# Optimization experiments

Hardware: AMD Instinct MI355X
Metric: run time of the kernel (lower is better)

Reference implementation:

```python
import jax, jax.numpy as jnp
import numpy as np

B, S, D, H = 8, 1024, 1024, 16
HD = D // H  # head_dim = 64


def setup_inputs() -> dict:
    key = jax.random.key(0)
    ks = jax.random.split(key, 5)
    scale = 1.0 / np.sqrt(D)
    return {
        "x": jax.random.normal(ks[0], (B, S, D), dtype=jnp.float32),
        "wq": jax.random.normal(ks[1], (D, D), dtype=jnp.float32) * scale,
        "wk": jax.random.normal(ks[2], (D, D), dtype=jnp.float32) * scale,
        "wv": jax.random.normal(ks[3], (D, D), dtype=jnp.float32) * scale,
        "wo": jax.random.normal(ks[4], (D, D), dtype=jnp.float32) * scale,
    }


def reference(x, wq, wk, wv, wo):
    b, s, d = x.shape
    # nn.Linear: y = x @ W.T  (weights stored [out, in])
    q = (x @ wq.T).reshape(b, s, H, HD).transpose(0, 2, 1, 3)  # [b,h,s,hd]
    k = (x @ wk.T).reshape(b, s, H, HD).transpose(0, 2, 1, 3)
    v = (x @ wv.T).reshape(b, s, H, HD).transpose(0, 2, 1, 3)
    scores = jnp.einsum("bhqd,bhkd->bhqk", q, k) / jnp.sqrt(jnp.float32(HD))
    attn = jax.nn.softmax(scores, axis=-1)  # dropout p=0.0 -> identity
    out = jnp.einsum("bhqk,bhkd->bhqd", attn, v)
    out = out.transpose(0, 2, 1, 3).reshape(b, s, d)
    return out @ wo.T
```

## Files before the change

kernel.cpp:

```cpp
#include <hip/hip_runtime.h>
#include <hip/hip_bf16.h>
#include <math.h>

#define BB 8
#define SS 1024
#define DD 1024
#define HH 16
#define HDIM 64
#define MM (BB * SS)
#define QSCALE 0.1803368801111204f

typedef __attribute__((ext_vector_type(8))) short s8v;
typedef __attribute__((ext_vector_type(4))) short s4v;
typedef __attribute__((ext_vector_type(4))) float f4v;

#define GLD16(g, l)                                                            \
  __builtin_amdgcn_global_load_lds(                                            \
      (const __attribute__((address_space(1))) void*)(g),                      \
      (__attribute__((address_space(3))) void*)(l), 16, 0, 0)

__device__ __forceinline__ unsigned short bf16_ru(float f) {
  return (unsigned short)((__float_as_uint(f) + 0x8000u) >> 16);
}

__device__ __forceinline__ unsigned bf16_pack2(float f0, float f1) {
#if __has_builtin(__builtin_amdgcn_perm)
  unsigned a = __float_as_uint(f0) + 0x8000u;
  unsigned b = __float_as_uint(f1) + 0x8000u;
  return __builtin_amdgcn_perm(b, a, 0x07060302u);
#else
  return (unsigned)bf16_ru(f0) | ((unsigned)bf16_ru(f1) << 16);
#endif
}

__device__ __forceinline__ float fast_exp2(float x) {
  return __builtin_amdgcn_exp2f(x);
}

__global__ void cast_all(const float* __restrict__ x, const float* __restrict__ wq,
                         const float* __restrict__ wk, const float* __restrict__ wv,
                         const float* __restrict__ wo, __hip_bfloat16* __restrict__ xb,
                         __hip_bfloat16* __restrict__ wqkvb,
                         __hip_bfloat16* __restrict__ wob) {
  int blk = blockIdx.x;
  const float* src;
  __hip_bfloat16* dst;
  int base;
  if (blk < 2048) {
    src = x; dst = xb; base = blk * 4096;
  } else if (blk < 2304) {
    src = wq; dst = wqkvb; base = (blk - 2048) * 4096;
  } else if (blk < 2560) {
    src = wk; dst = wqkvb + (1 << 20); base = (blk - 2304) * 4096;
  } else if (blk < 2816) {
    src = wv; dst = wqkvb + (2 << 20); base = (blk - 2560) * 4096;
  } else {
    src = wo; dst = wob; base = (blk - 2816) * 4096;
  }
#pragma unroll
  for (int it = 0; it < 4; ++it) {
    int idx = base + it * 1024 + threadIdx.x * 4;
    float4 f = *(const float4*)&src[idx];
    *(uint2*)&dst[idx] = uint2{bf16_pack2(f.x, f.y), bf16_pack2(f.z, f.w)};
  }
}

template <int MODE>
__global__ __launch_bounds__(256, (MODE == 0 ? 4 : 3)) void gemm_bt(
    const __hip_bfloat16* __restrict__ A, const __hip_bfloat16* __restrict__ Bm,
    float* __restrict__ Cf, __hip_bfloat16* __restrict__ Qo,
    __hip_bfloat16* __restrict__ Ko, __hip_bfloat16* __restrict__ Vt) {
  __shared__ __hip_bfloat16 sA[128 * 64];
  __shared__ __hip_bfloat16 sB[128 * 64];

  const int tid = threadIdx.x;
  const int wave = tid >> 6;
  const int lane = tid & 63;
  const int l15 = lane & 15;
  const int quad = lane >> 4;
  const int c8 = lane & 7;
  const int r8 = lane >> 3;

  const int m0 = blockIdx.y * 128;
  const int n0 = blockIdx.x * 128;
  const int wm = (wave >> 1) * 64;
  const int wn = (wave & 1) * 64;

  f4v acc[4][4];
#pragma unroll
  for (int i = 0; i < 4; ++i)
#pragma unroll
    for (int j = 0; j < 4; ++j) acc[i][j] = {0.f, 0.f, 0.f, 0.f};

  for (int kt = 0; kt < DD / 64; ++kt) {
    const int k0 = kt * 64;
    __syncthreads();
#pragma unroll
    for (int r = 0; r < 4; ++r) {
      int rb = r * 32 + wave * 8;
      int row = rb + r8;
      int scol = (c8 ^ (row & 7)) * 8;
      GLD16(A + (size_t)(m0 + row) * DD + k0 + scol, &sA[rb * 64]);
      GLD16(Bm + (size_t)(n0 + row) * DD + k0 + scol, &sB[rb * 64]);
    }
    __syncthreads();

#pragma unroll
    for (int kk = 0; kk < 2; ++kk) {
      s8v af[4], bf[4];
#pragma unroll
      for (int i = 0; i < 4; ++i)
        af[i] = *(const s8v*)&sA[(wm + i * 16 + l15) * 64 +
                                 (((kk * 4 + quad) ^ (l15 & 7)) * 8)];
#pragma unroll
      for (int j = 0; j < 4; ++j)
        bf[j] = *(const s8v*)&sB[(wn + j * 16 + l15) * 64 +
                                 (((kk * 4 + quad) ^ (l15 & 7)) * 8)];
#pragma unroll
      for (int i = 0; i < 4; ++i)
#pragma unroll
        for (int j = 0; j < 4; ++j)
          acc[i][j] = (MODE == 2)
                          ? __builtin_amdgcn_mfma_f32_16x16x32_bf16(af[i], bf[j],
                                                                    acc[i][j], 0, 0, 0)
                          : __builtin_amdgcn_mfma_f32_16x16x32_bf16(bf[j], af[i],
                                                                    acc[i][j], 0, 0, 0);
    }
  }

#pragma unroll
  for (int i = 0; i < 4; ++i) {
#pragma unroll
    for (int j = 0; j < 4; ++j) {
      if (MODE == 0) {
        const int s_abs = m0 + wm + i * 16 + l15;
        const int col = n0 + wn + j * 16 + quad * 4;
        const bool isQ = (n0 < 1024);
        const int hcol = col & 1023;
        const int h = hcol >> 6, hd = hcol & 63;
        const int b = s_abs >> 10, s = s_abs & 1023;
        const float scl = isQ ? QSCALE : 1.0f;
        __hip_bfloat16* dst = isQ ? Qo : Ko;
        *(uint2*)&dst[((size_t)(b * HH + h) * SS + s) * HDIM + hd] =
            uint2{bf16_pack2(acc[i][j][0] * scl, acc[i][j][1] * scl),
                  bf16_pack2(acc[i][j][2] * scl, acc[i][j][3] * scl)};
      } else if (MODE == 1) {
        const int s_abs = m0 + wm + i * 16 + l15;
        const int col = n0 + wn + j * 16 + quad * 4;
        float4 f4 = {acc[i][j][0], acc[i][j][1], acc[i][j][2], acc[i][j][3]};
        *(float4*)&Cf[(size_t)s_abs * DD + col] = f4;
      } else {
        const int rowb = m0 + wm + i * 16 + quad * 4;
        const int colb = n0 + wn + j * 16 + l15;
        const int h = colb >> 6, hd = colb & 63;
        const int b = rowb >> 10, s = rowb & 1023;
        *(uint2*)&Vt[((size_t)(b * HH + h) * HDIM + hd) * SS + s] =
            uint2{bf16_pack2(acc[i][j][0], acc[i][j][1]),
                  bf16_pack2(acc[i][j][2], acc[i][j][3])};
      }
    }
  }
}

#define KPLD 76
__global__ __launch_bounds__(256, 4) void attn_kernel(
    const __hip_bfloat16* __restrict__ Q, const __hip_bfloat16* __restrict__ K,
    const __hip_bfloat16* __restrict__ Vt, __hip_bfloat16* __restrict__ Oout) {
  __shared__ __hip_bfloat16 sK[64 * 64];
  __shared__ __hip_bfloat16 sVt[64 * 64];
  __shared__ unsigned short sP[4 * 32 * KPLD];

  const int tid = threadIdx.x;
  const int wave = tid >> 6;
  const int lane = tid & 63;
  const int l15 = lane & 15;
  const int quad = lane >> 4;
  const int c8 = lane & 7;
  const int r8 = lane >> 3;

  const int bh = blockIdx.x;
  const int q0 = blockIdx.y * 128;
  const size_t head = (size_t)bh * SS * HDIM;

  unsigned short* sPw = &sP[wave * 32 * KPLD];

  s8v qf[2][2];
#pragma unroll
  for (int mf = 0; mf < 2; ++mf) {
    int s = q0 + wave * 32 + mf * 16 + l15;
#pragma unroll
    for (int kk = 0; kk < 2; ++kk)
      qf[mf][kk] = *(const s8v*)&Q[head + (size_t)s * HDIM + kk * 32 + quad * 8];
  }

  s8v onesB;
#pragma unroll
  for (int j = 0; j < 8; ++j) onesB[j] = (short)0x3F80;

  f4v o[2][4];
  f4v lacc[2];
#pragma unroll
  for (int mf = 0; mf < 2; ++mf) {
    lacc[mf] = {0.f, 0.f, 0.f, 0.f};
#pragma unroll
    for (int f = 0; f < 4; ++f) o[mf][f] = {0.f, 0.f, 0.f, 0.f};
  }

  for (int kb = 0; kb < SS / 64; ++kb) {
    __syncthreads();
#pragma unroll
    for (int r = 0; r < 2; ++r) {
      int rb = r * 32 + wave * 8;
      int row = rb + r8;
      int sc8 = (c8 ^ (row & 7)) * 8;
      GLD16(&K[head + (size_t)(kb * 64 + row) * HDIM + sc8], &sK[rb * 64]);
      GLD16(&Vt[head + (size_t)row * SS + kb * 64 + sc8], &sVt[rb * 64]);
    }
    __syncthreads();

    f4v sc[2][4];
#pragma unroll
    for (int mf = 0; mf < 2; ++mf)
#pragma unroll
      for (int f = 0; f < 4; ++f) sc[mf][f] = {0.f, 0.f, 0.f, 0.f};
#pragma unroll
    for (int kk = 0; kk < 2; ++kk) {
#pragma unroll
      for (int f = 0; f < 4; ++f) {
        s8v kf = *(const s8v*)&sK[(f * 16 + l15) * 64 +
                                  (((kk * 4 + quad) ^ (l15 & 7)) * 8)];
#pragma unroll
        for (int mf = 0; mf < 2; ++mf)
          sc[mf][f] =
              __builtin_amdgcn_mfma_f32_16x16x32_bf16(kf, qf[mf][kk], sc[mf][f], 0, 0, 0);
      }
    }

#pragma unroll
    for (int mf = 0; mf < 2; ++mf)
#pragma unroll
      for (int f = 0; f < 4; ++f) {
        float p0 = fast_exp2(sc[mf][f][0]), p1 = fast_exp2(sc[mf][f][1]);
        float p2 = fast_exp2(sc[mf][f][2]), p3 = fast_exp2(sc[mf][f][3]);
        *(uint2*)&sPw[(mf * 16 + l15) * KPLD + f * 16 + quad * 4] =
            uint2{bf16_pack2(p0, p1), bf16_pack2(p2, p3)};
      }

#pragma unroll
    for (int kk = 0; kk < 2; ++kk) {
      s8v pf[2];
#pragma unroll
      for (int mf = 0; mf < 2; ++mf) {
        const unsigned short* p = &sPw[(mf * 16 + l15) * KPLD + kk * 32 + quad * 8];
        s4v lo = *(const s4v*)p;
        s4v hi = *(const s4v*)(p + 4);
        pf[mf] = __builtin_shufflevector(lo, hi, 0, 1, 2, 3, 4, 5, 6, 7);
        lacc[mf] = __builtin_amdgcn_mfma_f32_16x16x32_bf16(pf[mf], onesB, lacc[mf], 0, 0, 0);
      }
#pragma unroll
      for (int f = 0; f < 4; ++f) {
        s8v vf = *(const s8v*)&sVt[(f * 16 + l15) * 64 +
                                   (((kk * 4 + quad) ^ (l15 & 7)) * 8)];
#pragma unroll
        for (int mf = 0; mf < 2; ++mf)
          o[mf][f] =
              __builtin_amdgcn_mfma_f32_16x16x32_bf16(pf[mf], vf, o[mf][f], 0, 0, 0);
      }
    }
  }

  const int b = bh >> 4, h = bh & 15;
#pragma unroll
  for (int mf = 0; mf < 2; ++mf) {
    float rl[4];
#pragma unroll
    for (int r = 0; r < 4; ++r) rl[r] = 1.0f / lacc[mf][r];
#pragma unroll
    for (int f = 0; f < 4; ++f)
#pragma unroll
      for (int r = 0; r < 4; ++r) {
        int srow = q0 + wave * 32 + mf * 16 + quad * 4 + r;
        int col = h * HDIM + f * 16 + l15;
        ((unsigned short*)Oout)[(size_t)(b * SS + srow) * DD + col] =
            bf16_ru(o[mf][f][r] * rl[r]);
      }
  }
}

extern "C" void kernel_launch(void* const* d_in, const int* in_sizes, int n_in,
                              void* d_out, int out_size, void* d_ws, size_t ws_size,
                              hipStream_t stream) {
  const float* x = (const float*)d_in[0];
  const float* wq = (const float*)d_in[1];
  const float* wk = (const float*)d_in[2];
  const float* wv = (const float*)d_in[3];
  const float* wo = (const float*)d_in[4];

  char* ws = (char*)d_ws;
  __hip_bfloat16* xb = (__hip_bfloat16*)(ws);
  __hip_bfloat16* wqkvb = (__hip_bfloat16*)(ws + (16 << 20));
  __hip_bfloat16* wob = (__hip_bfloat16*)(ws + (22 << 20));
  __hip_bfloat16* qh = (__hip_bfloat16*)(ws + (24 << 20));
  __hip_bfloat16* kh = (__hip_bfloat16*)(ws + (40 << 20));
  __hip_bfloat16* vt = (__hip_bfloat16*)(ws + (56 << 20));
  __hip_bfloat16* attnO = (__hip_bfloat16*)(ws + (72 << 20));

  cast_all<<<3072, 256, 0, stream>>>(x, wq, wk, wv, wo, xb, wqkvb, wob);

  gemm_bt<0><<<dim3(16, 64), 256, 0, stream>>>(xb, wqkvb, nullptr, qh, kh, nullptr);
  gemm_bt<2><<<dim3(8, 64), 256, 0, stream>>>(xb, wqkvb + (2 << 20), nullptr,
                                              nullptr, nullptr, vt);

  attn_kernel<<<dim3(BB * HH, SS / 128), 256, 0, stream>>>(qh, kh, vt, attnO);

  gemm_bt<1><<<dim3(8, 64), 256, 0, stream>>>(attnO, wob, (float*)d_out, nullptr,
                                              nullptr, nullptr);
}
```

Baseline: 234.3 us.

## Stage GEMM epilogues through LDS, remap workgroups, widen attention P loads

The QKV and V-transpose GEMM epilogues now write bf16 tiles into swizzled LDS and then emit coalesced 16-byte global stores, instead of scattered 8-byte stores. Workgroup IDs are remapped so that consecutive blocks are spread across XCDs/tiles for better L2 locality. In attention, the P row pitch goes from 76 to 80 so each lane reads P with a single 16-byte load instead of two 8-byte loads, and s_setprio is raised around MFMA sections. The costs are an extra LDS round trip and barrier in the epilogue, plus possible LDS bank-conflict changes from the new padding.

```diff
diff --git a/kernel.cpp b/kernel.cpp
--- a/kernel.cpp
+++ b/kernel.cpp
@@ -70,8 +70,9 @@
     const __hip_bfloat16* __restrict__ A, const __hip_bfloat16* __restrict__ Bm,
     float* __restrict__ Cf, __hip_bfloat16* __restrict__ Qo,
     __hip_bfloat16* __restrict__ Ko, __hip_bfloat16* __restrict__ Vt) {
-  __shared__ __hip_bfloat16 sA[128 * 64];
-  __shared__ __hip_bfloat16 sB[128 * 64];
+  __shared__ __hip_bfloat16 smem[2][128 * 64];
+  __hip_bfloat16* sA = smem[0];
+  __hip_bfloat16* sB = smem[1];
 
   const int tid = threadIdx.x;
   const int wave = tid >> 6;
@@ -81,8 +82,13 @@
   const int c8 = lane & 7;
   const int r8 = lane >> 3;
 
-  const int m0 = blockIdx.y * 128;
-  const int n0 = blockIdx.x * 128;
+  constexpr int GX = (MODE == 0) ? 16 : 8;
+  constexpr int NWG = GX * 64;
+  const int id = blockIdx.y * GX + blockIdx.x;
+  const int nid = (id & 7) * (NWG / 8) + (id >> 3);
+  const int m0 = (nid / GX) * 128;
+  const int n0 = (nid % GX) * 128;
+
   const int wm = (wave >> 1) * 64;
   const int wn = (wave & 1) * 64;
 
@@ -128,41 +134,65 @@
     }
   }
 
-#pragma unroll
-  for (int i = 0; i < 4; ++i) {
-#pragma unroll
-    for (int j = 0; j < 4; ++j) {
-      if (MODE == 0) {
-        const int s_abs = m0 + wm + i * 16 + l15;
-        const int col = n0 + wn + j * 16 + quad * 4;
-        const bool isQ = (n0 < 1024);
-        const int hcol = col & 1023;
-        const int h = hcol >> 6, hd = hcol & 63;
-        const int b = s_abs >> 10, s = s_abs & 1023;
-        const float scl = isQ ? QSCALE : 1.0f;
-        __hip_bfloat16* dst = isQ ? Qo : Ko;
-        *(uint2*)&dst[((size_t)(b * HH + h) * SS + s) * HDIM + hd] =
-            uint2{bf16_pack2(acc[i][j][0] * scl, acc[i][j][1] * scl),
-                  bf16_pack2(acc[i][j][2] * scl, acc[i][j][3] * scl)};
-      } else if (MODE == 1) {
+  if constexpr (MODE == 1) {
+#pragma unroll
+    for (int i = 0; i < 4; ++i) {
+#pragma unroll
+      for (int j = 0; j < 4; ++j) {
         const int s_abs = m0 + wm + i * 16 + l15;
         const int col = n0 + wn + j * 16 + quad * 4;
         float4 f4 = {acc[i][j][0], acc[i][j][1], acc[i][j][2], acc[i][j][3]};
         *(float4*)&Cf[(size_t)s_abs * DD + col] = f4;
-      } else {
-        const int rowb = m0 + wm + i * 16 + quad * 4;
-        const int colb = n0 + wn + j * 16 + l15;
-        const int h = colb >> 6, hd = colb & 63;
-        const int b = rowb >> 10, s = rowb & 1023;
-        *(uint2*)&Vt[((size_t)(b * HH + h) * HDIM + hd) * SS + s] =
-            uint2{bf16_pack2(acc[i][j][0], acc[i][j][1]),
-                  bf16_pack2(acc[i][j][2], acc[i][j][3])};
-      }
-    }
-  }
-}
-
-#define KPLD 76
+      }
+    }
+  } else {
+    __syncthreads();
+    char* epc = (char*)smem + wave * 8192;
+    const float scl = (MODE == 0) ? ((n0 < 1024) ? QSCALE : 1.0f) : 1.0f;
+#pragma unroll
+    for (int i = 0; i < 4; ++i) {
+#pragma unroll
+      for (int j = 0; j < 4; ++j) {
+        const int r = (MODE == 0 ? i : j) * 16 + l15;
+        const int c0 = (MODE == 0 ? j : i) * 16 + quad * 4;
+        const int off = r * 128 + (((c0 >> 3) ^ (r & 7)) << 4) + ((c0 & 7) * 2);
+        *(uint2*)(epc + off) =
+            uint2{bf16_pack2(acc[i][j][0] * scl, acc[i][j][1] * scl),
+                  bf16_pack2(acc[i][j][2] * scl, acc[i][j][3] * scl)};
+      }
+    }
+    asm volatile("s_waitcnt lgkmcnt(0)" ::: "memory");
+    const int rr8 = lane >> 3;
+    const int ch = (lane & 7) ^ rr8;
+    if constexpr (MODE == 0) {
+      const bool isQ = (n0 < 1024);
+      const int h = ((n0 + wn) & 1023) >> 6;
+      const int sb = m0 + wm;
+      const int b = sb >> 10, s0 = sb & 1023;
+      __hip_bfloat16* dst =
+          (isQ ? Qo : Ko) + ((size_t)(b * HH + h) * SS + s0) * HDIM;
+#pragma unroll
+      for (int it = 0; it < 8; ++it) {
+        const int r = it * 8 + rr8;
+        uint4 vv = *(const uint4*)(epc + r * 128 + ch * 16);
+        *(uint4*)&dst[(size_t)r * HDIM + (lane & 7) * 8] = vv;
+      }
+    } else {
+      const int h = ((n0 + wn) & 1023) >> 6;
+      const int sb = m0 + wm;
+      const int b = sb >> 10, s0 = sb & 1023;
+      __hip_bfloat16* dst = Vt + (size_t)(b * HH + h) * HDIM * SS + s0;
+#pragma unroll
+      for (int it = 0; it < 8; ++it) {
+        const int r = it * 8 + rr8;
+        uint4 vv = *(const uint4*)(epc + r * 128 + ch * 16);
+        *(uint4*)&dst[(size_t)r * SS + (lane & 7) * 8] = vv;
+      }
+    }
+  }
+}
+
+#define KPLD 80
 __global__ __launch_bounds__(256, 4) void attn_kernel(
     const __hip_bfloat16* __restrict__ Q, const __hip_bfloat16* __restrict__ K,
     const __hip_bfloat16* __restrict__ Vt, __hip_bfloat16* __restrict__ Oout) {
@@ -223,6 +253,7 @@
     for (int mf = 0; mf < 2; ++mf)
 #pragma unroll
       for (int f = 0; f < 4; ++f) sc[mf][f] = {0.f, 0.f, 0.f, 0.f};
+    __builtin_amdgcn_s_setprio(1);
 #pragma unroll
     for (int kk = 0; kk < 2; ++kk) {
 #pragma unroll
@@ -235,6 +266,7 @@
               __builtin_amdgcn_mfma_f32_16x16x32_bf16(kf, qf[mf][kk], sc[mf][f], 0, 0, 0);
       }
     }
+    __builtin_amdgcn_s_setprio(0);
 
 #pragma unroll
     for (int mf = 0; mf < 2; ++mf)
@@ -246,15 +278,13 @@
             uint2{bf16_pack2(p0, p1), bf16_pack2(p2, p3)};
       }
 
+    __builtin_amdgcn_s_setprio(1);
 #pragma unroll
     for (int kk = 0; kk < 2; ++kk) {
       s8v pf[2];
 #pragma unroll
       for (int mf = 0; mf < 2; ++mf) {
-        const unsigned short* p = &sPw[(mf * 16 + l15) * KPLD + kk * 32 + quad * 8];
-        s4v lo = *(const s4v*)p;
-        s4v hi = *(const s4v*)(p + 4);
-        pf[mf] = __builtin_shufflevector(lo, hi, 0, 1, 2, 3, 4, 5, 6, 7);
+        pf[mf] = *(const s8v*)&sPw[(mf * 16 + l15) * KPLD + kk * 32 + quad * 8];
         lacc[mf] = __builtin_amdgcn_mfma_f32_16x16x32_bf16(pf[mf], onesB, lacc[mf], 0, 0, 0);
       }
 #pragma unroll
@@ -267,6 +297,7 @@
               __builtin_amdgcn_mfma_f32_16x16x32_bf16(pf[mf], vf, o[mf][f], 0, 0, 0);
       }
     }
+    __builtin_amdgcn_s_setprio(0);
   }
 
   const int b = bh >> 4, h = bh & 15;
```

Result: faster. 226.1 us (-3.5%).
